# Performance work log

Hardware: AMD Instinct MI355X
Metric: run time of the kernel (lower is better)

Reference implementation:

```python
import jax, jax.numpy as jnp
import numpy as np

B, C, T, V, D, H, KT = 64, 3, 256, 21, 128, 4, 9


def _adjacency():
    rng = np.random.default_rng(0)
    Araw = (rng.random((V, V)) < 0.3).astype(np.float32)
    Araw = np.maximum(Araw, Araw.T)
    np.fill_diagonal(Araw, 1.0)
    deg = Araw.sum(1)
    Anorm = Araw / np.sqrt(deg[:, None] * deg[None, :])  # D^-1/2 A D^-1/2
    return Araw.astype(np.float32), Anorm.astype(np.float32)


def setup_inputs() -> dict:
    key = jax.random.key(0)
    ks = jax.random.split(key, 24)
    g = lambda i, shape, sc=0.05: jax.random.normal(ks[i], shape, dtype=jnp.float32) * sc
    Araw, Anorm = _adjacency()
    return {
        'x': jax.random.normal(ks[0], (B, C, T, V), dtype=jnp.float32),
        'coord_w': g(1, (C, D)), 'coord_b': g(2, (D,)),
        'joint_emb': g(3, (V, D)),
        'graph_bias': jnp.asarray(Araw),  # nn.Parameter(A.clone().float())
        'wq': g(4, (D, D)), 'bq': g(5, (D,)),
        'wk': g(6, (D, D)), 'bk': g(7, (D,)),
        'wv': g(8, (D, D)), 'bv': g(9, (D,)),
        'wo': g(10, (D, D)), 'bo': g(11, (D,)),
        'gcn_w1': g(12, (D, D)), 'gcn_b1': g(13, (D,)),
        'tcn_w1': g(14, (D, D, KT, 1)), 'tcn_b1': g(15, (D,)),
        'gcn_w2': g(16, (D, D)), 'gcn_b2': g(17, (D,)),
        'tcn_w2': g(18, (D, D, KT, 1)), 'tcn_b2': g(19, (D,)),
        'A': jnp.asarray(Anorm),  # fixed normalized adjacency buffer
    }


def _stgcn(x, A, gw, gb, tw, tb):
    # x: [B, D, T, V]; spatial graph conv then temporal conv, residual.
    res = x
    y = jnp.einsum('bctv,vw->bctw', x, A)              # neighbor aggregation
    y = jnp.einsum('bctv,dc->bdtv', y, gw) + gb[None, :, None, None]
    y = jax.nn.relu(y)
    y = jax.lax.conv_general_dilated(
        y, tw, window_strides=(1, 1), padding=((KT // 2, KT // 2), (0, 0)),
        dimension_numbers=('NCHW', 'OIHW', 'NCHW'))     # temporal conv, kernel 9
    y = y + tb[None, :, None, None]
    return jax.nn.relu(y + res)


def reference(x, coord_w, coord_b, joint_emb, graph_bias, wq, bq, wk, bk, wv, bv,
              wo, bo, gcn_w1, gcn_b1, tcn_w1, tcn_b1, gcn_w2, gcn_b2, tcn_w2,
              tcn_b2, A):
    b, c, t, v = x.shape
    d = coord_w.shape[1]
    dh = d // H
    scale = jnp.float32(1.0 / np.sqrt(dh))
    coords = x.transpose(0, 2, 3, 1).reshape(b * t, v, c)      # [N, V, 3]
    feat = coords @ coord_w + coord_b + joint_emb              # LearnedJointEncoding
    q = (feat @ wq + bq).reshape(-1, v, H, dh)
    k = (feat @ wk + bk).reshape(-1, v, H, dh)
    val = (feat @ wv + bv).reshape(-1, v, H, dh)
    scores = jnp.einsum('nihd,njhd->nhij', q, k) * scale + graph_bias[None, None]
    attn = jax.nn.softmax(scores, axis=-1)                     # [N, H, V, V]
    out = jnp.einsum('nhij,njhd->nihd', attn, val).reshape(-1, v, d)
    feat = out @ wo + bo
    feat = feat.reshape(b, t, v, d).transpose(0, 3, 1, 2)       # [B, D, T, V]
    feat = _stgcn(feat, A, gcn_w1, gcn_b1, tcn_w1, tcn_b1)
    feat = _stgcn(feat, A, gcn_w2, gcn_b2, tcn_w2, tcn_b2)
    return feat, attn
```

## Files before the change

### kernel.cpp

```cpp
#include <hip/hip_runtime.h>
#include <hip/hip_bf16.h>

typedef __hip_bfloat16 bf16;
typedef __attribute__((ext_vector_type(8))) short short8v;
typedef __attribute__((ext_vector_type(4))) float float4v;

#define BB   64
#define CC   3
#define TLEN 256
#define VJ   21
#define DM   128
#define NH   4
#define DH   32
#define KT   9
#define NFR  (BB*TLEN)
#define MTOK (NFR*VJ)
#define NIN  22

__device__ __forceinline__ float b2f(bf16 x){ return __bfloat162float(x); }
__device__ __forceinline__ bf16  f2b(float x){ return __float2bfloat16(x); }
__device__ __forceinline__ float hb2f(short s){ return __uint_as_float(((unsigned)(unsigned short)s) << 16); }
__device__ __forceinline__ float lo16(unsigned u){ return __uint_as_float(u << 16); }
__device__ __forceinline__ float hi16(unsigned u){ return __uint_as_float(u & 0xffff0000u); }

__global__ void detect_dtype(const void* __restrict__ xin, int nus, int* __restrict__ flag){
  const unsigned short* u = (const unsigned short*)xin;
  int lim = nus < 65536 ? nus : 65536;
  int bad = 0;
  for (int k = threadIdx.x; k < lim; k += 256){
    float f = __uint_as_float(((unsigned)u[k]) << 16);
    if (!(fabsf(f) < 1e6f)) bad = 1;
  }
  if (bad) atomicOr(flag, 1);
}

struct ConvArgs { const void* src[NIN]; int off[NIN+1]; };

__global__ void convert_inputs(ConvArgs a, bf16* __restrict__ dst,
                               const int* __restrict__ flag, int total){
  int i = blockIdx.x*256 + threadIdx.x;
  if (i >= total) return;
  bool isf32 = (*flag != 0);
  int k = 0;
  while (i >= a.off[k+1]) ++k;
  int j = i - a.off[k];
  float v;
  if (isf32) v = ((const float*)a.src[k])[j];
  else       v = __uint_as_float(((unsigned)((const unsigned short*)a.src[k])[j]) << 16);
  dst[i] = f2b(v);
}

__global__ void prep_weights(const bf16* __restrict__ wq, const bf16* __restrict__ wk,
                             const bf16* __restrict__ wv, const bf16* __restrict__ wo,
                             const bf16* __restrict__ tw1, const bf16* __restrict__ tw2,
                             bf16* __restrict__ wqT, bf16* __restrict__ wkT,
                             bf16* __restrict__ wvT, bf16* __restrict__ woT,
                             bf16* __restrict__ twT1, bf16* __restrict__ twT2){
  int i = blockIdx.x*256 + threadIdx.x;
  if (i < DM*DM){
    int d = i >> 7, e = i & 127;
    wqT[i] = wq[e*DM + d];
    wkT[i] = wk[e*DM + d];
    wvT[i] = wv[e*DM + d];
    woT[i] = wo[e*DM + d];
  }
  if (i < KT*DM*DM){
    int c = i & 127; int d = (i >> 7) & 127; int tap = i >> 14;
    twT1[i] = tw1[(d*DM + c)*KT + tap];
    twT2[i] = tw2[(d*DM + c)*KT + tap];
  }
}

__global__ __launch_bounds__(256) void encode_kernel(const bf16* __restrict__ x,
                                                     const bf16* __restrict__ cw,
                                                     const bf16* __restrict__ cb,
                                                     const bf16* __restrict__ je,
                                                     bf16* __restrict__ feat){
  int idx = blockIdx.x*256 + threadIdx.x;
  if (idx >= MTOK*16) return;
  int d0 = (idx & 15) * 8;
  int n  = idx >> 4;
  int v  = n % VJ; int t = (n / VJ) % TLEN; int b = n / (VJ*TLEN);
  float xs[CC];
  #pragma unroll
  for (int c = 0; c < CC; ++c)
    xs[c] = b2f(x[((size_t)(b*CC + c)*TLEN + t)*VJ + v]);
  short8v cwv[CC];
  #pragma unroll
  for (int c = 0; c < CC; ++c)
    cwv[c] = *reinterpret_cast<const short8v*>(cw + c*DM + d0);
  short8v cbv = *reinterpret_cast<const short8v*>(cb + d0);
  short8v jev = *reinterpret_cast<const short8v*>(je + v*DM + d0);
  short8v out;
  #pragma unroll
  for (int e = 0; e < 8; ++e){
    float acc = hb2f(cbv[e]) + hb2f(jev[e]);
    #pragma unroll
    for (int c = 0; c < CC; ++c) acc = fmaf(xs[c], hb2f(cwv[c][e]), acc);
    bf16 h = f2b(acc);
    out[e] = *reinterpret_cast<short*>(&h);
  }
  *reinterpret_cast<short8v*>(feat + (size_t)n*DM + d0*1) = out;
}

__global__ __launch_bounds__(512) void qkv_gemm(const bf16* __restrict__ A,
                                                const bf16* __restrict__ BtQ,
                                                const bf16* __restrict__ BtK,
                                                const bf16* __restrict__ BtV,
                                                const bf16* __restrict__ bq,
                                                const bf16* __restrict__ bk,
                                                const bf16* __restrict__ bv,
                                                bf16* __restrict__ Oq,
                                                bf16* __restrict__ Ok,
                                                bf16* __restrict__ Ov){
  __shared__ short8v lds[128*16];
  const int tid = threadIdx.x;
  const int r0  = blockIdx.x*128;
  for (int i = tid; i < 128*16; i += 512){
    int row = i >> 4, c0 = i & 15;
    lds[row*16 + (c0 ^ (row & 7))] = *reinterpret_cast<const short8v*>(A + ((size_t)r0 + row)*DM + c0*8);
  }
  __syncthreads();
  const int lane = tid & 63;
  const int wid  = tid >> 6;
  const int rbase = (wid >> 2) * 64;
  const int nt0   = (wid & 3) * 2;
  const int l15 = lane & 15, l4 = lane >> 4;
  #pragma unroll
  for (int w = 0; w < 3; ++w){
    const bf16* Bt  = (w==0) ? BtQ : (w==1) ? BtK : BtV;
    const bf16* bia = (w==0) ? bq  : (w==1) ? bk  : bv;
    bf16*       Out = (w==0) ? Oq  : (w==1) ? Ok  : Ov;
    short8v breg[2][4];
    #pragma unroll
    for (int ntl = 0; ntl < 2; ++ntl)
      #pragma unroll
      for (int ks = 0; ks < 4; ++ks)
        breg[ntl][ks] = *reinterpret_cast<const short8v*>(Bt + ((nt0+ntl)*16 + l15)*DM + ks*32 + l4*8);
    float4v acc[4][2];
    #pragma unroll
    for (int rt = 0; rt < 4; ++rt){ acc[rt][0] = (float4v){0,0,0,0}; acc[rt][1] = (float4v){0,0,0,0}; }
    #pragma unroll
    for (int rt = 0; rt < 4; ++rt){
      const int ldsRow = rbase + rt*16 + l15;
      #pragma unroll
      for (int ks = 0; ks < 4; ++ks){
        short8v a = lds[ldsRow*16 + ((ks*4 + l4) ^ (ldsRow & 7))];
        acc[rt][0] = __builtin_amdgcn_mfma_f32_16x16x32_bf16(a, breg[0][ks], acc[rt][0], 0,0,0);
        acc[rt][1] = __builtin_amdgcn_mfma_f32_16x16x32_bf16(a, breg[1][ks], acc[rt][1], 0,0,0);
      }
    }
    #pragma unroll
    for (int rt = 0; rt < 4; ++rt)
      #pragma unroll
      for (int ntl = 0; ntl < 2; ++ntl){
        int col = (nt0+ntl)*16 + l15;
        float bvv = b2f(bia[col]);
        #pragma unroll
        for (int j = 0; j < 4; ++j)
          Out[(size_t)(r0 + rbase + rt*16 + l4*4 + j)*DM + col] = f2b(acc[rt][ntl][j] + bvv);
      }
  }
}

template<int NTAPS, bool RELU, bool RESID>
__global__ __launch_bounds__(512, 4) void conv_gemm(const bf16* __restrict__ A,
                                                    const bf16* __restrict__ Bt,
                                                    const bf16* __restrict__ bias,
                                                    const bf16* resid,
                                                    bf16* Cout){
  constexpr int HALO = (NTAPS/2)*VJ;
  constexpr int ROWS = 128 + 2*HALO;
  __shared__ short8v lds[ROWS*16];
  const int tid = threadIdx.x;
  const int r0  = blockIdx.x*128;
  for (int i = tid; i < ROWS*16; i += 512){
    int row = i >> 4, c0 = i & 15;
    long tok = (long)r0 - HALO + row;
    if (tok < 0) tok = 0;
    if (tok > MTOK-1) tok = MTOK-1;
    lds[row*16 + (c0 ^ (row & 7))] = *reinterpret_cast<const short8v*>(A + tok*DM + c0*8);
  }
  __syncthreads();
  const int lane = tid & 63;
  const int wid  = tid >> 6;
  const int rbase = (wid >> 2) * 64;
  const int nt0   = (wid & 3) * 2;
  const int l15 = lane & 15, l4 = lane >> 4;
  int trow[4];
  #pragma unroll
  for (int rt = 0; rt < 4; ++rt)
    trow[rt] = ((r0 + rbase + rt*16 + l15) / VJ) % TLEN;
  float4v acc[4][2];
  #pragma unroll
  for (int rt = 0; rt < 4; ++rt){ acc[rt][0] = (float4v){0,0,0,0}; acc[rt][1] = (float4v){0,0,0,0}; }

  const bf16* bptr = Bt + (nt0*16 + l15)*DM + l4*8;
  short8v bcur[2][4], bnxt[2][4];
  #pragma unroll
  for (int ntl = 0; ntl < 2; ++ntl)
    #pragma unroll
    for (int ks = 0; ks < 4; ++ks)
      bcur[ntl][ks] = *reinterpret_cast<const short8v*>(bptr + ntl*16*DM + ks*32);

  #pragma unroll
  for (int tap = 0; tap < NTAPS; ++tap){
    if (tap + 1 < NTAPS){
      const bf16* bp = bptr + (size_t)(tap+1)*DM*DM;
      #pragma unroll
      for (int ntl = 0; ntl < 2; ++ntl)
        #pragma unroll
        for (int ks = 0; ks < 4; ++ks)
          bnxt[ntl][ks] = *reinterpret_cast<const short8v*>(bp + ntl*16*DM + ks*32);
    }
    const int dt = tap - NTAPS/2;
    #pragma unroll
    for (int rt = 0; rt < 4; ++rt){
      bool valid = true;
      if (NTAPS > 1){
        int ts = trow[rt] + dt;
        valid = (ts >= 0) && (ts < TLEN);
      }
      const int ldsRow = rbase + rt*16 + l15 + HALO + dt*VJ;
      #pragma unroll
      for (int ks = 0; ks < 4; ++ks){
        short8v a = lds[ldsRow*16 + ((ks*4 + l4) ^ (ldsRow & 7))];
        if (NTAPS > 1 && !valid) a = (short8v){0,0,0,0,0,0,0,0};
        acc[rt][0] = __builtin_amdgcn_mfma_f32_16x16x32_bf16(a, bcur[0][ks], acc[rt][0], 0,0,0);
        acc[rt][1] = __builtin_amdgcn_mfma_f32_16x16x32_bf16(a, bcur[1][ks], acc[rt][1], 0,0,0);
      }
    }
    if (tap + 1 < NTAPS){
      #pragma unroll
      for (int ntl = 0; ntl < 2; ++ntl)
        #pragma unroll
        for (int ks = 0; ks < 4; ++ks)
          bcur[ntl][ks] = bnxt[ntl][ks];
    }
  }
  #pragma unroll
  for (int rt = 0; rt < 4; ++rt){
    #pragma unroll
    for (int ntl = 0; ntl < 2; ++ntl){
      int col = (nt0+ntl)*16 + l15;
      float bv = b2f(bias[col]);
      #pragma unroll
      for (int j = 0; j < 4; ++j){
        size_t idx = (size_t)(r0 + rbase + rt*16 + l4*4 + j)*DM + col;
        float val = acc[rt][ntl][j] + bv;
        if (RESID) val += b2f(resid[idx]);
        if (RELU) val = fmaxf(val, 0.f);
        Cout[idx] = f2b(val);
      }
    }
  }
}

__global__ __launch_bounds__(256) void attn_core(const bf16* __restrict__ Q,
                                                 const bf16* __restrict__ K,
                                                 const bf16* __restrict__ V,
                                                 const bf16* __restrict__ gbias,
                                                 float* __restrict__ attn_out,
                                                 bf16* __restrict__ ao_out){
  const int n = blockIdx.x;
  const int tid = threadIdx.x;
  __shared__ bf16 skv[3][VJ][136];
  __shared__ float sc[NH*VJ*VJ];
  __shared__ float rmax[NH*VJ], rinv[NH*VJ];
  __shared__ bf16 sgb[VJ*VJ];

  for (int i = tid; i < VJ*VJ; i += 256) sgb[i] = gbias[i];
  for (int i = tid; i < 3*VJ*16; i += 256){
    int c0 = i & 15; int v = (i >> 4) % VJ; int w = i / (16*VJ);
    const bf16* src = (w==0 ? Q : (w==1 ? K : V)) + ((size_t)n*VJ + v)*DM + c0*8;
    *reinterpret_cast<short8v*>(&skv[w][v][c0*8]) = *reinterpret_cast<const short8v*>(src);
  }
  __syncthreads();
  const float scale = 0.17677669529663687f;
  for (int idx = tid; idx < NH*VJ*VJ; idx += 256){
    int j = idx % VJ, i2 = (idx/VJ) % VJ, h = idx/(VJ*VJ);
    const unsigned* qr = reinterpret_cast<const unsigned*>(&skv[0][i2][h*DH]);
    const unsigned* kr = reinterpret_cast<const unsigned*>(&skv[1][j][h*DH]);
    float a = 0.f;
    #pragma unroll
    for (int p = 0; p < DH/2; ++p){
      unsigned qa = qr[p], ka = kr[p];
      a = fmaf(lo16(qa), lo16(ka), a);
      a = fmaf(hi16(qa), hi16(ka), a);
    }
    sc[idx] = a*scale + b2f(sgb[i2*VJ + j]);
  }
  __syncthreads();
  for (int r = tid; r < NH*VJ; r += 256){
    float m = -1e30f;
    for (int j = 0; j < VJ; ++j) m = fmaxf(m, sc[r*VJ + j]);
    float s = 0.f;
    for (int j = 0; j < VJ; ++j) s += __expf(sc[r*VJ + j] - m);
    rmax[r] = m; rinv[r] = 1.0f/s;
  }
  __syncthreads();
  for (int idx = tid; idx < NH*VJ*VJ; idx += 256){
    int r = idx / VJ;
    float e = __expf(sc[idx] - rmax[r]) * rinv[r];
    sc[idx] = e;
    attn_out[(size_t)n*(NH*VJ*VJ) + idx] = e;
  }
  __syncthreads();
  unsigned* aoU = reinterpret_cast<unsigned*>(ao_out);
  for (int i = tid; i < VJ*(DM/2); i += 256){
    int q2 = i & 63; int v = i >> 6;
    int d0 = q2*2; int h = d0 >> 5;
    const float* pr = &sc[(h*VJ + v)*VJ];
    float a0 = 0.f, a1 = 0.f;
    #pragma unroll
    for (int j = 0; j < VJ; ++j){
      unsigned va = *reinterpret_cast<const unsigned*>(&skv[2][j][d0]);
      float p = pr[j];
      a0 = fmaf(p, lo16(va), a0);
      a1 = fmaf(p, hi16(va), a1);
    }
    bf16 b0 = f2b(a0), b1 = f2b(a1);
    unsigned u0 = *reinterpret_cast<unsigned short*>(&b0);
    unsigned u1 = *reinterpret_cast<unsigned short*>(&b1);
    aoU[((size_t)n*VJ + v)*(DM/2) + q2] = u0 | (u1 << 16);
  }
}

__global__ __launch_bounds__(256) void agg_kernel(const bf16* __restrict__ fin,
                                                  const bf16* __restrict__ An,
                                                  bf16* __restrict__ aout){
  const int n = blockIdx.x;
  const int tid = threadIdx.x;
  __shared__ bf16 sx[VJ][136];
  __shared__ float sA[VJ*VJ];
  for (int i = tid; i < VJ*VJ; i += 256) sA[i] = b2f(An[i]);
  for (int i = tid; i < VJ*16; i += 256){
    int c0 = i & 15, v = i >> 4;
    *reinterpret_cast<short8v*>(&sx[v][c0*8]) =
      *reinterpret_cast<const short8v*>(fin + ((size_t)n*VJ + v)*DM + c0*8);
  }
  __syncthreads();
  for (int i = tid; i < VJ*16; i += 256){
    int c0 = i & 15, w = i >> 4;
    float acc[8] = {0,0,0,0,0,0,0,0};
    #pragma unroll
    for (int u = 0; u < VJ; ++u){
      float a = sA[u*VJ + w];
      short8v xv = *reinterpret_cast<const short8v*>(&sx[u][c0*8]);
      #pragma unroll
      for (int e = 0; e < 8; ++e) acc[e] = fmaf(a, hb2f(xv[e]), acc[e]);
    }
    short8v out;
    #pragma unroll
    for (int e = 0; e < 8; ++e){ bf16 h = f2b(acc[e]); out[e] = *reinterpret_cast<short*>(&h); }
    *reinterpret_cast<short8v*>(aout + ((size_t)n*VJ + w)*DM + c0*8) = out;
  }
}

__global__ __launch_bounds__(256) void transpose_out(const bf16* __restrict__ fin,
                                                     float* __restrict__ fout){
  const int bid = blockIdx.x;
  const int b   = bid >> 5;
  const int rem = bid & 31;
  const int t0  = (rem >> 2) * 32;
  const int d0  = (rem & 3) * 32;
  __shared__ bf16 tile[32][VJ][33];
  const int tid = threadIdx.x;
  for (int idx = tid; idx < 32*VJ*32; idx += 256){
    int dl = idx & 31;
    int v  = (idx >> 5) % VJ;
    int tl = idx / (32*VJ);
    tile[tl][v][dl] = fin[((size_t)(b*TLEN + t0 + tl)*VJ + v)*DM + d0 + dl];
  }
  __syncthreads();
  for (int idx = tid; idx < 32*VJ*32; idx += 256){
    int j  = idx % (32*VJ);
    int dl = idx / (32*VJ);
    int tl = j / VJ, v = j % VJ;
    fout[((size_t)(b*DM + d0 + dl)*TLEN + t0 + tl)*VJ + v] = b2f(tile[tl][v][dl]);
  }
}

extern "C" void kernel_launch(void* const* d_in, const int* in_sizes, int n_in,
                              void* d_out, int out_size, void* d_ws, size_t ws_size,
                              hipStream_t stream){
  const size_t featElems = (size_t)MTOK*DM;
  float* outf    = (float*)d_out;
  float* attnOut = outf + featElems;
  bf16* qbuf = (bf16*)d_out;
  bf16* kbuf = qbuf + featElems;

  char* wp = (char*)d_ws;
  auto alloc = [&](size_t bytes)->char*{ char* p = wp; wp += (bytes + 15) & ~(size_t)15; return p; };
  int*  flag = (int*)alloc(16);
  ConvArgs ca; int total = 0;
  for (int i = 0; i < NIN; ++i){ ca.src[i] = d_in[i]; ca.off[i] = total; total += in_sizes[i]; }
  ca.off[NIN] = total;
  bf16* cin   = (bf16*)alloc((size_t)total*2);
  bf16* wqT   = (bf16*)alloc(DM*DM*2);
  bf16* wkT   = (bf16*)alloc(DM*DM*2);
  bf16* wvT   = (bf16*)alloc(DM*DM*2);
  bf16* woT   = (bf16*)alloc(DM*DM*2);
  bf16* twT1  = (bf16*)alloc(KT*DM*DM*2);
  bf16* twT2  = (bf16*)alloc(KT*DM*DM*2);
  bf16* featA = (bf16*)alloc(featElems*2);
  bf16* bufV  = (bf16*)alloc(featElems*2);
  if ((size_t)(wp - (char*)d_ws) > ws_size) return;

  const bf16* x    = cin + ca.off[0];
  const bf16* cw   = cin + ca.off[1];
  const bf16* cb   = cin + ca.off[2];
  const bf16* je   = cin + ca.off[3];
  const bf16* gbias= cin + ca.off[4];
  const bf16* wq   = cin + ca.off[5];
  const bf16* bq   = cin + ca.off[6];
  const bf16* wk   = cin + ca.off[7];
  const bf16* bk   = cin + ca.off[8];
  const bf16* wv   = cin + ca.off[9];
  const bf16* bv   = cin + ca.off[10];
  const bf16* wo   = cin + ca.off[11];
  const bf16* bo   = cin + ca.off[12];
  const bf16* gw1  = cin + ca.off[13];
  const bf16* gb1  = cin + ca.off[14];
  const bf16* tw1  = cin + ca.off[15];
  const bf16* tb1  = cin + ca.off[16];
  const bf16* gw2  = cin + ca.off[17];
  const bf16* gb2  = cin + ca.off[18];
  const bf16* tw2  = cin + ca.off[19];
  const bf16* tb2  = cin + ca.off[20];
  const bf16* An   = cin + ca.off[21];

  const int GB = MTOK/128;
  hipMemsetAsync(flag, 0, sizeof(int), stream);
  detect_dtype<<<1, 256, 0, stream>>>(d_in[0], in_sizes[0], flag);
  convert_inputs<<<(total + 255)/256, 256, 0, stream>>>(ca, cin, flag, total);
  prep_weights<<<(KT*DM*DM + 255)/256, 256, 0, stream>>>(wq, wk, wv, wo, tw1, tw2,
                                                         wqT, wkT, wvT, woT, twT1, twT2);
  encode_kernel<<<(MTOK*16 + 255)/256, 256, 0, stream>>>(x, cw, cb, je, featA);
  qkv_gemm<<<GB, 512, 0, stream>>>(featA, wqT, wkT, wvT, bq, bk, bv, qbuf, kbuf, bufV);
  attn_core<<<NFR, 256, 0, stream>>>(qbuf, kbuf, bufV, gbias, attnOut, featA);
  conv_gemm<1,false,false><<<GB, 512, 0, stream>>>(featA, woT, bo, nullptr, bufV);
  agg_kernel<<<NFR, 256, 0, stream>>>(bufV, An, qbuf);
  conv_gemm<1,true,false><<<GB, 512, 0, stream>>>(qbuf, gw1, gb1, nullptr, kbuf);
  conv_gemm<9,true,true><<<GB, 512, 0, stream>>>(kbuf, twT1, tb1, bufV, bufV);
  agg_kernel<<<NFR, 256, 0, stream>>>(bufV, An, qbuf);
  conv_gemm<1,true,false><<<GB, 512, 0, stream>>>(qbuf, gw2, gb2, nullptr, kbuf);
  conv_gemm<9,true,true><<<GB, 512, 0, stream>>>(kbuf, twT2, tb2, bufV, bufV);
  transpose_out<<<BB*(TLEN/32)*(DM/32), 256, 0, stream>>>(bufV, outf);
}
```

Before: 1.316 ms.

## Fuse joint encoding into QKV GEMM and output projection into attention

The coordinate and joint-embedding encoding is now computed directly into the QKV GEMM's LDS tile, so the separate encode kernel and its feature round trip through global memory are gone. The attention kernel now stages its per-frame head outputs in swizzled LDS and applies the output projection with MFMA before writing features. This removes two launches and two full activation write/read passes. In exchange, every attention block re-reads the 128x128 output-projection weight from global/L2, pads the 21 joints to 32 MFMA rows, and uses more LDS per block, which may lower occupancy.

```diff
diff --git a/kernel.cpp b/kernel.cpp
--- a/kernel.cpp
+++ b/kernel.cpp
@@ -71,39 +71,10 @@
   }
 }
 
-__global__ __launch_bounds__(256) void encode_kernel(const bf16* __restrict__ x,
-                                                     const bf16* __restrict__ cw,
-                                                     const bf16* __restrict__ cb,
-                                                     const bf16* __restrict__ je,
-                                                     bf16* __restrict__ feat){
-  int idx = blockIdx.x*256 + threadIdx.x;
-  if (idx >= MTOK*16) return;
-  int d0 = (idx & 15) * 8;
-  int n  = idx >> 4;
-  int v  = n % VJ; int t = (n / VJ) % TLEN; int b = n / (VJ*TLEN);
-  float xs[CC];
-  #pragma unroll
-  for (int c = 0; c < CC; ++c)
-    xs[c] = b2f(x[((size_t)(b*CC + c)*TLEN + t)*VJ + v]);
-  short8v cwv[CC];
-  #pragma unroll
-  for (int c = 0; c < CC; ++c)
-    cwv[c] = *reinterpret_cast<const short8v*>(cw + c*DM + d0);
-  short8v cbv = *reinterpret_cast<const short8v*>(cb + d0);
-  short8v jev = *reinterpret_cast<const short8v*>(je + v*DM + d0);
-  short8v out;
-  #pragma unroll
-  for (int e = 0; e < 8; ++e){
-    float acc = hb2f(cbv[e]) + hb2f(jev[e]);
-    #pragma unroll
-    for (int c = 0; c < CC; ++c) acc = fmaf(xs[c], hb2f(cwv[c][e]), acc);
-    bf16 h = f2b(acc);
-    out[e] = *reinterpret_cast<short*>(&h);
-  }
-  *reinterpret_cast<short8v*>(feat + (size_t)n*DM + d0*1) = out;
-}
-
-__global__ __launch_bounds__(512) void qkv_gemm(const bf16* __restrict__ A,
+__global__ __launch_bounds__(512) void qkv_gemm(const bf16* __restrict__ x,
+                                                const bf16* __restrict__ cw,
+                                                const bf16* __restrict__ cb,
+                                                const bf16* __restrict__ je,
                                                 const bf16* __restrict__ BtQ,
                                                 const bf16* __restrict__ BtK,
                                                 const bf16* __restrict__ BtV,
@@ -114,11 +85,38 @@
                                                 bf16* __restrict__ Ok,
                                                 bf16* __restrict__ Ov){
   __shared__ short8v lds[128*16];
+  __shared__ float sxf[128][4];
   const int tid = threadIdx.x;
   const int r0  = blockIdx.x*128;
+  {
+    int tok = tid >> 2, c = tid & 3;
+    if (tok < 128 && c < 3){
+      int n = r0 + tok;
+      int v = n % VJ; int t = (n / VJ) % TLEN; int b = n / (VJ*TLEN);
+      sxf[tok][c] = b2f(x[((size_t)(b*CC + c)*TLEN + t)*VJ + v]);
+    }
+  }
+  __syncthreads();
   for (int i = tid; i < 128*16; i += 512){
     int row = i >> 4, c0 = i & 15;
-    lds[row*16 + (c0 ^ (row & 7))] = *reinterpret_cast<const short8v*>(A + ((size_t)r0 + row)*DM + c0*8);
+    int n = r0 + row; int v = n % VJ;
+    short8v cw0 = *reinterpret_cast<const short8v*>(cw + 0*DM + c0*8);
+    short8v cw1 = *reinterpret_cast<const short8v*>(cw + 1*DM + c0*8);
+    short8v cw2 = *reinterpret_cast<const short8v*>(cw + 2*DM + c0*8);
+    short8v cbv = *reinterpret_cast<const short8v*>(cb + c0*8);
+    short8v jev = *reinterpret_cast<const short8v*>(je + v*DM + c0*8);
+    float x0 = sxf[row][0], x1 = sxf[row][1], x2 = sxf[row][2];
+    short8v out;
+    #pragma unroll
+    for (int e = 0; e < 8; ++e){
+      float f = hb2f(cbv[e]) + hb2f(jev[e]);
+      f = fmaf(x0, hb2f(cw0[e]), f);
+      f = fmaf(x1, hb2f(cw1[e]), f);
+      f = fmaf(x2, hb2f(cw2[e]), f);
+      bf16 h = f2b(f);
+      out[e] = *reinterpret_cast<short*>(&h);
+    }
+    lds[row*16 + (c0 ^ (row & 7))] = out;
   }
   __syncthreads();
   const int lane = tid & 63;
@@ -260,14 +258,17 @@
                                                  const bf16* __restrict__ K,
                                                  const bf16* __restrict__ V,
                                                  const bf16* __restrict__ gbias,
+                                                 const bf16* __restrict__ woT,
+                                                 const bf16* __restrict__ bo,
                                                  float* __restrict__ attn_out,
-                                                 bf16* __restrict__ ao_out){
+                                                 bf16* __restrict__ feat_out){
   const int n = blockIdx.x;
   const int tid = threadIdx.x;
   __shared__ bf16 skv[3][VJ][136];
   __shared__ float sc[NH*VJ*VJ];
   __shared__ float rmax[NH*VJ], rinv[NH*VJ];
   __shared__ bf16 sgb[VJ*VJ];
+  __shared__ short8v sao[32*16];
 
   for (int i = tid; i < VJ*VJ; i += 256) sgb[i] = gbias[i];
   for (int i = tid; i < 3*VJ*16; i += 256){
@@ -306,7 +307,6 @@
     attn_out[(size_t)n*(NH*VJ*VJ) + idx] = e;
   }
   __syncthreads();
-  unsigned* aoU = reinterpret_cast<unsigned*>(ao_out);
   for (int i = tid; i < VJ*(DM/2); i += 256){
     int q2 = i & 63; int v = i >> 6;
     int d0 = q2*2; int h = d0 >> 5;
@@ -322,7 +322,43 @@
     bf16 b0 = f2b(a0), b1 = f2b(a1);
     unsigned u0 = *reinterpret_cast<unsigned short*>(&b0);
     unsigned u1 = *reinterpret_cast<unsigned short*>(&b1);
-    aoU[((size_t)n*VJ + v)*(DM/2) + q2] = u0 | (u1 << 16);
+    unsigned* lp = reinterpret_cast<unsigned*>(&sao[v*16 + ((q2 >> 2) ^ (v & 7))]);
+    lp[q2 & 3] = u0 | (u1 << 16);
+  }
+  __syncthreads();
+  const int lane = tid & 63;
+  const int wid  = tid >> 6;
+  const int l15 = lane & 15, l4 = lane >> 4;
+  float4v acc[2][2];
+  #pragma unroll
+  for (int mt = 0; mt < 2; ++mt){ acc[mt][0] = (float4v){0,0,0,0}; acc[mt][1] = (float4v){0,0,0,0}; }
+  #pragma unroll
+  for (int ks = 0; ks < 4; ++ks){
+    short8v bfr[2];
+    #pragma unroll
+    for (int ct = 0; ct < 2; ++ct)
+      bfr[ct] = *reinterpret_cast<const short8v*>(woT + (wid*32 + ct*16 + l15)*DM + ks*32 + l4*8);
+    #pragma unroll
+    for (int mt = 0; mt < 2; ++mt){
+      int row = mt*16 + l15;
+      short8v a = sao[row*16 + ((ks*4 + l4) ^ (row & 7))];
+      acc[mt][0] = __builtin_amdgcn_mfma_f32_16x16x32_bf16(a, bfr[0], acc[mt][0], 0,0,0);
+      acc[mt][1] = __builtin_amdgcn_mfma_f32_16x16x32_bf16(a, bfr[1], acc[mt][1], 0,0,0);
+    }
+  }
+  #pragma unroll
+  for (int mt = 0; mt < 2; ++mt){
+    #pragma unroll
+    for (int ct = 0; ct < 2; ++ct){
+      int col = wid*32 + ct*16 + l15;
+      float bov = b2f(bo[col]);
+      #pragma unroll
+      for (int j = 0; j < 4; ++j){
+        int row = mt*16 + l4*4 + j;
+        if (row < VJ)
+          feat_out[((size_t)n*VJ + row)*DM + col] = f2b(acc[mt][ct][j] + bov);
+      }
+    }
   }
 }
 
@@ -436,15 +472,14 @@
   convert_inputs<<<(total + 255)/256, 256, 0, stream>>>(ca, cin, flag, total);
   prep_weights<<<(KT*DM*DM + 255)/256, 256, 0, stream>>>(wq, wk, wv, wo, tw1, tw2,
                                                          wqT, wkT, wvT, woT, twT1, twT2);
-  encode_kernel<<<(MTOK*16 + 255)/256, 256, 0, stream>>>(x, cw, cb, je, featA);
-  qkv_gemm<<<GB, 512, 0, stream>>>(featA, wqT, wkT, wvT, bq, bk, bv, qbuf, kbuf, bufV);
-  attn_core<<<NFR, 256, 0, stream>>>(qbuf, kbuf, bufV, gbias, attnOut, featA);
-  conv_gemm<1,false,false><<<GB, 512, 0, stream>>>(featA, woT, bo, nullptr, bufV);
-  agg_kernel<<<NFR, 256, 0, stream>>>(bufV, An, qbuf);
+  qkv_gemm<<<GB, 512, 0, stream>>>(x, cw, cb, je, wqT, wkT, wvT, bq, bk, bv,
+                                   qbuf, kbuf, bufV);
+  attn_core<<<NFR, 256, 0, stream>>>(qbuf, kbuf, bufV, gbias, woT, bo, attnOut, featA);
+  agg_kernel<<<NFR, 256, 0, stream>>>(featA, An, qbuf);
   conv_gemm<1,true,false><<<GB, 512, 0, stream>>>(qbuf, gw1, gb1, nullptr, kbuf);
-  conv_gemm<9,true,true><<<GB, 512, 0, stream>>>(kbuf, twT1, tb1, bufV, bufV);
-  agg_kernel<<<NFR, 256, 0, stream>>>(bufV, An, qbuf);
+  conv_gemm<9,true,true><<<GB, 512, 0, stream>>>(kbuf, twT1, tb1, featA, featA);
+  agg_kernel<<<NFR, 256, 0, stream>>>(featA, An, qbuf);
   conv_gemm<1,true,false><<<GB, 512, 0, stream>>>(qbuf, gw2, gb2, nullptr, kbuf);
-  conv_gemm<9,true,true><<<GB, 512, 0, stream>>>(kbuf, twT2, tb2, bufV, bufV);
-  transpose_out<<<BB*(TLEN/32)*(DM/32), 256, 0, stream>>>(bufV, outf);
-}
+  conv_gemm<9,true,true><<<GB, 512, 0, stream>>>(kbuf, twT2, tb2, featA, featA);
+  transpose_out<<<BB*(TLEN/32)*(DM/32), 256, 0, stream>>>(featA, outf);
+}
```

After: 1.306 ms. Within noise of the previous version (-0.8%).
